# Optimization experiments

Measured on AMD Instinct MI355X. Metric: run time of the kernel, lower is better.

Reference implementation:

```python
import jax, jax.numpy as jnp
import numpy as np

N, D, C = 4096, 512, 100
EPS = 1e-8


def setup_inputs() -> dict:
    key = jax.random.key(0)
    k1, k2 = jax.random.split(key)
    X = jax.random.normal(k1, (N, D), dtype=jnp.float32)
    # torch.rand -> uniform [0, 1), shape (1, hiddensize, classes)
    grp = jax.random.uniform(k2, (1, D, C), dtype=jnp.float32)
    return {"X": X, "grp": grp}


def reference(X, grp):
    # L1 distance of each sample to each class prototype: [N, D, 1] - [1, D, C] -> sum over D -> [N, C]
    l1 = jnp.abs(X[:, :, None] - grp).sum(axis=1)
    norm = jax.nn.softmax(-l1, axis=1)  # Softmin over classes

    # Cosine similarity between X [N, D] and prototypes grp[0] [D, C] -> [N, C]
    g = grp[0]
    dot = X @ g  # [N, C]
    xn = jnp.sqrt(jnp.sum(X * X, axis=1, keepdims=True))      # [N, 1]
    gn = jnp.sqrt(jnp.sum(g * g, axis=0, keepdims=True))      # [1, C]
    cs = dot / jnp.maximum(xn * gn, EPS)

    confidence = jnp.max(cs, axis=1, keepdims=True)  # [N, 1]
    confusion = jax.nn.softmax(cs, axis=1)           # [N, C]
    return confidence * confusion * norm
```

## Files before the change

kernel.cpp:

```cpp
#include <hip/hip_runtime.h>

typedef float v2f __attribute__((ext_vector_type(2)));

#define D_DIM 512
#define C_CLS 100
#define SAMP 2
#define NT 256

__global__ __launch_bounds__(NT, 6) void cls_kernel(const float* __restrict__ X,
                                                    const float* __restrict__ grp,
                                                    float* __restrict__ out) {
    __shared__ float4 pA[SAMP][8][25];
    __shared__ float4 pB[SAMP][8][25];
    __shared__ float4 pG[8][25];
    __shared__ float redA[SAMP][25];
    __shared__ float redB[SAMP][25];
    __shared__ float xsqs[SAMP];

    const int t = threadIdx.x;
    const int n0 = blockIdx.x * SAMP;
    const float* xb = X + (size_t)n0 * D_DIM;

    if (t < 32 * SAMP) {
        const int r = t >> 5, j = t & 31;
        float v = 0.f;
#pragma unroll
        for (int k = 0; k < 4; ++k) {
            float4 a = *(const float4*)&xb[(size_t)r * D_DIM + j * 4 + k * 128];
            v += a.x * a.x + a.y * a.y + a.z * a.z + a.w * a.w;
        }
#pragma unroll
        for (int m = 16; m > 0; m >>= 1) v += __shfl_xor(v, m, 32);
        if (j == 0) xsqs[r] = v;
    }

    const bool act = (t < 200);
    const int dq = t / 25;
    const int cq = t - dq * 25;

    float l1[SAMP][4];
    v2f dtl[SAMP], dth[SAMP];
    v2f gsql = {0.f, 0.f}, gsqh = {0.f, 0.f};
#pragma unroll
    for (int i = 0; i < SAMP; ++i) {
        dtl[i] = (v2f){0.f, 0.f};
        dth[i] = (v2f){0.f, 0.f};
#pragma unroll
        for (int j = 0; j < 4; ++j) l1[i][j] = 0.f;
    }

    if (act) {
        const float* gp = grp + cq * 4;
#pragma unroll 2
        for (int j = 0; j < 16; ++j) {
            const int d4 = j * 32 + dq * 4;
            float xr[SAMP][4];
#pragma unroll
            for (int si = 0; si < SAMP; ++si)
                *(float4*)&xr[si][0] = *(const float4*)&xb[si * D_DIM + d4];
#pragma unroll
            for (int k = 0; k < 4; ++k) {
                float4 g4 = *(const float4*)&gp[(d4 + k) * C_CLS];
                v2f glo = {g4.x, g4.y};
                v2f ghi = {g4.z, g4.w};
                gsql += glo * glo;
                gsqh += ghi * ghi;
#pragma unroll
                for (int si = 0; si < SAMP; ++si) {
                    float x = xr[si][k];
                    v2f x2 = {x, x};
                    v2f el = x2 - glo;
                    v2f eh = x2 - ghi;
                    l1[si][0] += fabsf(el.x);
                    l1[si][1] += fabsf(el.y);
                    l1[si][2] += fabsf(eh.x);
                    l1[si][3] += fabsf(eh.y);
                    dtl[si] += x2 * glo;
                    dth[si] += x2 * ghi;
                }
            }
        }
#pragma unroll
        for (int si = 0; si < SAMP; ++si) {
            pA[si][dq][cq] = float4{l1[si][0], l1[si][1], l1[si][2], l1[si][3]};
            pB[si][dq][cq] = float4{dtl[si].x, dtl[si].y, dth[si].x, dth[si].y};
        }
        pG[dq][cq] = float4{gsql.x, gsql.y, gsqh.x, gsqh.y};
    }
    __syncthreads();

    const int s  = t / 25;
    const int c2 = t - s * 25;
    const bool act2 = (t < 25 * SAMP);

    float l1c[4] = {0.f, 0.f, 0.f, 0.f};
    float dtc[4] = {0.f, 0.f, 0.f, 0.f};
    float gsc[4] = {0.f, 0.f, 0.f, 0.f};
    if (act2) {
#pragma unroll
        for (int q = 0; q < 8; ++q) {
            float4 a = pA[s][q][c2];
            float4 b = pB[s][q][c2];
            float4 c = pG[q][c2];
            l1c[0] += a.x; l1c[1] += a.y; l1c[2] += a.z; l1c[3] += a.w;
            dtc[0] += b.x; dtc[1] += b.y; dtc[2] += b.z; dtc[3] += b.w;
            gsc[0] += c.x; gsc[1] += c.y; gsc[2] += c.z; gsc[3] += c.w;
        }
    }

    float cs[4] = {0.f, 0.f, 0.f, 0.f};
    if (act2) {
        float xq = xsqs[s];
#pragma unroll
        for (int c = 0; c < 4; ++c)
            cs[c] = dtc[c] / fmaxf(sqrtf(xq * gsc[c]), 1e-8f);
        redA[s][c2] = fminf(fminf(l1c[0], l1c[1]), fminf(l1c[2], l1c[3]));
        redB[s][c2] = fmaxf(fmaxf(cs[0], cs[1]), fmaxf(cs[2], cs[3]));
    }
    __syncthreads();

    float minl1 = 0.f, maxcs = 0.f;
    if (act2) {
        minl1 = redA[s][0];
        maxcs = redB[s][0];
        for (int k = 1; k < 25; ++k) {
            minl1 = fminf(minl1, redA[s][k]);
            maxcs = fmaxf(maxcs, redB[s][k]);
        }
    }
    __syncthreads();

    if (act2) {
        redA[s][c2] = __expf(minl1 - l1c[0]) + __expf(minl1 - l1c[1]) +
                      __expf(minl1 - l1c[2]) + __expf(minl1 - l1c[3]);
        redB[s][c2] = __expf(cs[0] - maxcs) + __expf(cs[1] - maxcs) +
                      __expf(cs[2] - maxcs) + __expf(cs[3] - maxcs);
    }
    __syncthreads();

    if (act2) {
        float s1 = 0.f, s2 = 0.f;
        for (int k = 0; k < 25; ++k) { s1 += redA[s][k]; s2 += redB[s][k]; }
        float f = maxcs / (s1 * s2);
        float4 o;
        o.x = f * __expf(cs[0] - maxcs) * __expf(minl1 - l1c[0]);
        o.y = f * __expf(cs[1] - maxcs) * __expf(minl1 - l1c[1]);
        o.z = f * __expf(cs[2] - maxcs) * __expf(minl1 - l1c[2]);
        o.w = f * __expf(cs[3] - maxcs) * __expf(minl1 - l1c[3]);
        *(float4*)&out[(size_t)(n0 + s) * C_CLS + c2 * 4] = o;
    }
}

extern "C" void kernel_launch(void* const* d_in, const int* in_sizes, int n_in,
                              void* d_out, int out_size, void* d_ws, size_t ws_size,
                              hipStream_t stream) {
    const float* X   = (const float*)d_in[0];
    const float* grp = (const float*)d_in[1];
    float* out = (float*)d_out;
    (void)d_ws; (void)ws_size;

    cls_kernel<<<4096 / SAMP, NT, 0, stream>>>(X, grp, out);
}
```

Measured before the change: 35.73 us.

## Precompute prototype norms in separate kernel, raise samples per block, shuffle-reduce partials

Moves the per-class squared-norm computation of grp into a small pre-kernel that writes to workspace, so each block no longer recomputes it. Doubles samples per block to 4 so each grp load serves more samples. Remaps threads so the 8 D-slices of a class sit in adjacent lanes and are reduced with warp shuffles instead of shared-memory partials, with one spare thread group computing the X row norms. Costs an extra kernel launch, higher register pressure from the larger per-thread accumulators, and half as many blocks.

```diff
diff --git a/kernel.cpp b/kernel.cpp
--- a/kernel.cpp
+++ b/kernel.cpp
@@ -4,15 +4,41 @@
 
 #define D_DIM 512
 #define C_CLS 100
-#define SAMP 2
+#define SAMP 4
 #define NT 256
 
-__global__ __launch_bounds__(NT, 6) void cls_kernel(const float* __restrict__ X,
+__global__ __launch_bounds__(128) void gsq_kernel(const float* __restrict__ grp,
+                                                  float* __restrict__ ws) {
+    __shared__ float4 red[128];
+    const int t = threadIdx.x;
+    const int cb = blockIdx.x * 4;
+    float4 acc = {0.f, 0.f, 0.f, 0.f};
+    for (int d = t; d < D_DIM; d += 128) {
+        float4 g = *(const float4*)&grp[d * C_CLS + cb];
+        acc.x = fmaf(g.x, g.x, acc.x);
+        acc.y = fmaf(g.y, g.y, acc.y);
+        acc.z = fmaf(g.z, g.z, acc.z);
+        acc.w = fmaf(g.w, g.w, acc.w);
+    }
+    red[t] = acc;
+    __syncthreads();
+    for (int off = 64; off > 0; off >>= 1) {
+        if (t < off) {
+            float4 a = red[t], b = red[t + off];
+            a.x += b.x; a.y += b.y; a.z += b.z; a.w += b.w;
+            red[t] = a;
+        }
+        __syncthreads();
+    }
+    if (t == 0) *(float4*)&ws[cb] = red[0];
+}
+
+__global__ __launch_bounds__(NT, 5) void cls_kernel(const float* __restrict__ X,
                                                     const float* __restrict__ grp,
+                                                    const float* __restrict__ gsq,
                                                     float* __restrict__ out) {
-    __shared__ float4 pA[SAMP][8][25];
-    __shared__ float4 pB[SAMP][8][25];
-    __shared__ float4 pG[8][25];
+    __shared__ float4 pL1[SAMP][25];
+    __shared__ float4 pDT[SAMP][25];
     __shared__ float redA[SAMP][25];
     __shared__ float redB[SAMP][25];
     __shared__ float xsqs[SAMP];
@@ -20,27 +46,26 @@
     const int t = threadIdx.x;
     const int n0 = blockIdx.x * SAMP;
     const float* xb = X + (size_t)n0 * D_DIM;
+    const int cq = t >> 3;
+    const int dq = t & 7;
 
-    if (t < 32 * SAMP) {
-        const int r = t >> 5, j = t & 31;
-        float v = 0.f;
-#pragma unroll
-        for (int k = 0; k < 4; ++k) {
-            float4 a = *(const float4*)&xb[(size_t)r * D_DIM + j * 4 + k * 128];
-            v += a.x * a.x + a.y * a.y + a.z * a.z + a.w * a.w;
+    if (cq == 25) {
+        const int l = t & 7, si = l >> 1, half = l & 1;
+        const float* xr = xb + si * D_DIM + half * 256;
+        v2f acc = {0.f, 0.f};
+        for (int d4 = 0; d4 < 256; d4 += 4) {
+            float4 a = *(const float4*)&xr[d4];
+            v2f u = {a.x, a.y}, w = {a.z, a.w};
+            acc += u * u;
+            acc += w * w;
         }
-#pragma unroll
-        for (int m = 16; m > 0; m >>= 1) v += __shfl_xor(v, m, 32);
-        if (j == 0) xsqs[r] = v;
+        float v = acc.x + acc.y;
+        v += __shfl_xor(v, 1);
+        if (half == 0) xsqs[si] = v;
     }
-
-    const bool act = (t < 200);
-    const int dq = t / 25;
-    const int cq = t - dq * 25;
 
     float l1[SAMP][4];
     v2f dtl[SAMP], dth[SAMP];
-    v2f gsql = {0.f, 0.f}, gsqh = {0.f, 0.f};
 #pragma unroll
     for (int i = 0; i < SAMP; ++i) {
         dtl[i] = (v2f){0.f, 0.f};
@@ -49,9 +74,9 @@
         for (int j = 0; j < 4; ++j) l1[i][j] = 0.f;
     }
 
-    if (act) {
+    if (cq < 25) {
         const float* gp = grp + cq * 4;
-#pragma unroll 2
+#pragma unroll 1
         for (int j = 0; j < 16; ++j) {
             const int d4 = j * 32 + dq * 4;
             float xr[SAMP][4];
@@ -61,10 +86,7 @@
 #pragma unroll
             for (int k = 0; k < 4; ++k) {
                 float4 g4 = *(const float4*)&gp[(d4 + k) * C_CLS];
-                v2f glo = {g4.x, g4.y};
-                v2f ghi = {g4.z, g4.w};
-                gsql += glo * glo;
-                gsqh += ghi * ghi;
+                v2f glo = {g4.x, g4.y}, ghi = {g4.z, g4.w};
 #pragma unroll
                 for (int si = 0; si < SAMP; ++si) {
                     float x = xr[si][k];
@@ -81,39 +103,43 @@
             }
         }
 #pragma unroll
-        for (int si = 0; si < SAMP; ++si) {
-            pA[si][dq][cq] = float4{l1[si][0], l1[si][1], l1[si][2], l1[si][3]};
-            pB[si][dq][cq] = float4{dtl[si].x, dtl[si].y, dth[si].x, dth[si].y};
+        for (int m = 1; m <= 4; m <<= 1) {
+#pragma unroll
+            for (int si = 0; si < SAMP; ++si) {
+#pragma unroll
+                for (int c = 0; c < 4; ++c) l1[si][c] += __shfl_xor(l1[si][c], m);
+                dtl[si].x += __shfl_xor(dtl[si].x, m);
+                dtl[si].y += __shfl_xor(dtl[si].y, m);
+                dth[si].x += __shfl_xor(dth[si].x, m);
+                dth[si].y += __shfl_xor(dth[si].y, m);
+            }
         }
-        pG[dq][cq] = float4{gsql.x, gsql.y, gsqh.x, gsqh.y};
+        if (dq == 0) {
+#pragma unroll
+            for (int si = 0; si < SAMP; ++si) {
+                pL1[si][cq] = float4{l1[si][0], l1[si][1], l1[si][2], l1[si][3]};
+                pDT[si][cq] = float4{dtl[si].x, dtl[si].y, dth[si].x, dth[si].y};
+            }
+        }
     }
     __syncthreads();
 
     const int s  = t / 25;
     const int c2 = t - s * 25;
-    const bool act2 = (t < 25 * SAMP);
+    const bool act2 = (t < 100);
 
     float l1c[4] = {0.f, 0.f, 0.f, 0.f};
-    float dtc[4] = {0.f, 0.f, 0.f, 0.f};
-    float gsc[4] = {0.f, 0.f, 0.f, 0.f};
+    float cs[4]  = {0.f, 0.f, 0.f, 0.f};
     if (act2) {
-#pragma unroll
-        for (int q = 0; q < 8; ++q) {
-            float4 a = pA[s][q][c2];
-            float4 b = pB[s][q][c2];
-            float4 c = pG[q][c2];
-            l1c[0] += a.x; l1c[1] += a.y; l1c[2] += a.z; l1c[3] += a.w;
-            dtc[0] += b.x; dtc[1] += b.y; dtc[2] += b.z; dtc[3] += b.w;
-            gsc[0] += c.x; gsc[1] += c.y; gsc[2] += c.z; gsc[3] += c.w;
-        }
-    }
-
-    float cs[4] = {0.f, 0.f, 0.f, 0.f};
-    if (act2) {
+        float4 a = pL1[s][c2];
+        float4 b = pDT[s][c2];
+        float4 gq = *(const float4*)&gsq[c2 * 4];
         float xq = xsqs[s];
-#pragma unroll
-        for (int c = 0; c < 4; ++c)
-            cs[c] = dtc[c] / fmaxf(sqrtf(xq * gsc[c]), 1e-8f);
+        l1c[0] = a.x; l1c[1] = a.y; l1c[2] = a.z; l1c[3] = a.w;
+        cs[0] = b.x / fmaxf(sqrtf(xq * gq.x), 1e-8f);
+        cs[1] = b.y / fmaxf(sqrtf(xq * gq.y), 1e-8f);
+        cs[2] = b.z / fmaxf(sqrtf(xq * gq.z), 1e-8f);
+        cs[3] = b.w / fmaxf(sqrtf(xq * gq.w), 1e-8f);
         redA[s][c2] = fminf(fminf(l1c[0], l1c[1]), fminf(l1c[2], l1c[3]));
         redB[s][c2] = fmaxf(fmaxf(cs[0], cs[1]), fmaxf(cs[2], cs[3]));
     }
@@ -157,7 +183,8 @@
     const float* X   = (const float*)d_in[0];
     const float* grp = (const float*)d_in[1];
     float* out = (float*)d_out;
-    (void)d_ws; (void)ws_size;
+    float* ws  = (float*)d_ws;
 
-    cls_kernel<<<4096 / SAMP, NT, 0, stream>>>(X, grp, out);
+    gsq_kernel<<<25, 128, 0, stream>>>(grp, ws);
+    cls_kernel<<<4096 / SAMP, NT, 0, stream>>>(X, grp, ws, out);
 }
```

After: 63.61 us. +78.0%, slower.
